# Optimization experiments

Hardware: AMD Instinct MI355X
Metric: run time of the kernel (lower is better)

## Reference

```python
import jax, jax.numpy as jnp
import numpy as np

TEMPERATURE = 0.07
EPS = 1e-8  # torch CosineSimilarity eps


def setup_inputs() -> dict:
    key = jax.random.key(0)
    k1, k2, k3 = jax.random.split(key, 3)
    N, D = 8192, 512
    features = jax.random.normal(k1, (N, D), dtype=jnp.float32)
    positive_mask = jax.random.randint(k2, (N, N), 0, 2, dtype=jnp.int32)
    negative_mask = jax.random.randint(k3, (N, N), 0, 2, dtype=jnp.int32)
    return {"features": features, "positive_mask": positive_mask, "negative_mask": negative_mask}


def reference(features, positive_mask, negative_mask):
    N = positive_mask.shape[0]
    self_contrast = 1.0 - jnp.eye(N, dtype=features.dtype)  # zero diagonal
    pos = positive_mask.astype(features.dtype) * self_contrast  # [N, N]
    neg = negative_mask.astype(features.dtype) * self_contrast  # [N, N]

    # cosine similarity via normalized matmul (same math as broadcasted CosineSimilarity)
    norm = jnp.maximum(jnp.linalg.norm(features, axis=1, keepdims=True), EPS)
    fn = features / norm  # [N, D]
    sim = jnp.matmul(fn, fn.T) / TEMPERATURE  # [N, N]

    logits_max = jax.lax.stop_gradient(jnp.max(sim, axis=1, keepdims=True))
    e = jnp.exp(sim - logits_max)  # [N, N]

    positives = e * pos
    log_neg_sum = jnp.log(jnp.sum(e * neg, axis=1, keepdims=True))  # [N, 1]
    log_prob = positives - log_neg_sum  # [N, N] (faithful to source: exp-masked, not log)

    cardinal = jnp.sum(pos, axis=1)
    cardinal = jnp.where(cardinal == 0, 1.0, cardinal)
    log_prob_sum = jnp.sum(log_prob * pos, axis=1)
    loss = -log_prob_sum / cardinal
    return jnp.mean(loss)
```

## Files before the change

kernel.cpp:

```cpp
#include <hip/hip_runtime.h>
#include <hip/hip_bf16.h>
#include <math.h>

#define NN 8192
#define DD 512
#define INV_T 14.285714285714286f

typedef __attribute__((ext_vector_type(8))) short s16x8;
typedef __attribute__((ext_vector_type(4))) float f32x4;
typedef __attribute__((ext_vector_type(4))) int   i32x4;

__device__ __forceinline__ unsigned short f32_to_bf16(float f) {
  unsigned int u = __float_as_uint(f);
  u += 0x7FFFu + ((u >> 16) & 1u);
  return (unsigned short)(u >> 16);
}

__device__ __forceinline__ void async16(const void* g, void* l) {
  __builtin_amdgcn_global_load_lds((__attribute__((address_space(1))) void*)(void*)g,
                                   (__attribute__((address_space(3))) void*)l,
                                   16, 0, 0);
}

__global__ __launch_bounds__(256) void normalize_kernel(const float* __restrict__ f,
                                                        unsigned short* __restrict__ fnb) {
  const int wave = threadIdx.x >> 6;
  const int lane = threadIdx.x & 63;
  const int row  = blockIdx.x * 4 + wave;
  const float* src = f + (size_t)row * DD + lane * 8;
  float4 v0 = *(const float4*)src;
  float4 v1 = *(const float4*)(src + 4);
  float ss = v0.x*v0.x + v0.y*v0.y + v0.z*v0.z + v0.w*v0.w
           + v1.x*v1.x + v1.y*v1.y + v1.z*v1.z + v1.w*v1.w;
  #pragma unroll
  for (int o = 32; o; o >>= 1) ss += __shfl_xor(ss, o);
  const float r = 1.0f / fmaxf(sqrtf(ss), 1e-8f);
  ushort4 a, b;
  a.x = f32_to_bf16(v0.x * r); a.y = f32_to_bf16(v0.y * r);
  a.z = f32_to_bf16(v0.z * r); a.w = f32_to_bf16(v0.w * r);
  b.x = f32_to_bf16(v1.x * r); b.y = f32_to_bf16(v1.y * r);
  b.z = f32_to_bf16(v1.z * r); b.w = f32_to_bf16(v1.w * r);
  unsigned short* dst = fnb + (size_t)row * DD + lane * 8;
  *(ushort4*)dst = a;
  *(ushort4*)(dst + 4) = b;
}

__global__ __launch_bounds__(256, 3) void fused_kernel(const unsigned short* __restrict__ fnb,
                                                       const int* __restrict__ posm,
                                                       const int* __restrict__ negm,
                                                       float* __restrict__ Spos,
                                                       float* __restrict__ Sneg,
                                                       float* __restrict__ Pcnt) {
  const int bid = blockIdx.x;
  int bi = (int)(64.5 - sqrt(64.5 * 64.5 - 2.0 * (double)bid));
  while (64 * bi - bi * (bi - 1) / 2 > bid) --bi;
  while (64 * (bi + 1) - (bi + 1) * bi / 2 <= bid) ++bi;
  const int bj = bi + (bid - (64 * bi - bi * (bi - 1) / 2));
  const int I = bi * 128;
  const int J = bj * 128;
  const bool offdiag = (bi != bj);

  const int tid  = threadIdx.x;
  const int wave = tid >> 6;
  const int lane = tid & 63;
  const int wm = wave >> 1;
  const int wn = wave & 1;
  const int q   = lane >> 4;
  const int c16 = lane & 15;

  __shared__ alignas(16) unsigned short lA[128 * 32];
  __shared__ alignas(16) unsigned short lB[128 * 32];
  __shared__ float sacc[2][128][3];
  for (int t = tid; t < 2 * 128 * 3; t += 256) ((float*)sacc)[t] = 0.f;

  f32x4 acc[4][4];
  const f32x4 z4 = {0.f, 0.f, 0.f, 0.f};
  #pragma unroll
  for (int mt = 0; mt < 4; ++mt)
    #pragma unroll
    for (int nt = 0; nt < 4; ++nt) acc[mt][nt] = z4;

  for (int kk = 0; kk < DD / 32; ++kk) {
    const int k0 = kk * 32;
    #pragma unroll
    for (int c = 0; c < 2; ++c) {
      const int fidx = tid + c * 256;
      const int L    = fidx >> 2;
      const int p    = fidx & 3;
      const int csrc = (p ^ ((L >> 1) & 3)) & 3;
      async16(fnb + (size_t)(I + L) * DD + k0 + csrc * 8, (char*)lA + fidx * 16);
      const int gB = 4 * (L & 31) + (L >> 5);
      async16(fnb + (size_t)(J + gB) * DD + k0 + csrc * 8, (char*)lB + fidx * 16);
    }
    __syncthreads();

    s16x8 aF[4], bF[4];
    #pragma unroll
    for (int t = 0; t < 4; ++t) {
      const int arow = wm * 64 + t * 16 + c16;
      const int apos = (q ^ ((arow >> 1) & 3)) & 3;
      aF[t] = *(const s16x8*)((const char*)lA + arow * 64 + apos * 16);
      const int Lb = (wn * 16 + c16) | (t << 5);
      const int bpos = (q ^ ((Lb >> 1) & 3)) & 3;
      bF[t] = *(const s16x8*)((const char*)lB + Lb * 64 + bpos * 16);
    }
    #pragma unroll
    for (int mt = 0; mt < 4; ++mt)
      #pragma unroll
      for (int nt = 0; nt < 4; ++nt)
        acc[mt][nt] = __builtin_amdgcn_mfma_f32_16x16x32_bf16(aF[mt], bF[nt], acc[mt][nt], 0, 0, 0);
    __syncthreads();
  }

  #pragma unroll
  for (int mt = 0; mt < 4; ++mt)
    #pragma unroll
    for (int nt = 0; nt < 4; ++nt)
      #pragma unroll
      for (int r = 0; r < 4; ++r)
        acc[mt][nt][r] = __expf(acc[mt][nt][r] * INV_T - INV_T);

  const bool hasdiag = (bi == bj) && (wm == wn);
  const int cb = wn * 64 + 4 * c16;

  #pragma unroll
  for (int mt = 0; mt < 4; ++mt) {
    const int rl = wm * 64 + mt * 16 + q * 4;
    i32x4 pv[4], nv[4];
    #pragma unroll
    for (int r = 0; r < 4; ++r) {
      const size_t off = (size_t)(I + rl + r) * NN + J + cb;
      pv[r] = __builtin_nontemporal_load((const i32x4*)(posm + off));
      nv[r] = __builtin_nontemporal_load((const i32x4*)(negm + off));
    }
    #pragma unroll
    for (int r = 0; r < 4; ++r) {
      float dsp = 0.f, dsn = 0.f, dpc = 0.f;
      #pragma unroll
      for (int nt = 0; nt < 4; ++nt) {
        float pf = (float)pv[r][nt];
        float nf = (float)nv[r][nt];
        if (hasdiag && (rl + r == cb + nt)) { pf = 0.f; nf = 0.f; }
        const float e = acc[mt][nt][r];
        dsp = fmaf(e, pf, dsp);
        dsn = fmaf(e, nf, dsn);
        dpc += pf;
      }
      #pragma unroll
      for (int o = 1; o <= 8; o <<= 1) {
        dsp += __shfl_xor(dsp, o);
        dsn += __shfl_xor(dsn, o);
        dpc += __shfl_xor(dpc, o);
      }
      if (c16 == 0) {
        atomicAdd(&sacc[0][rl + r][0], dsp);
        atomicAdd(&sacc[0][rl + r][1], dsn);
        atomicAdd(&sacc[0][rl + r][2], dpc);
      }
    }
  }

  if (offdiag) {
    #pragma unroll
    for (int nt = 0; nt < 4; ++nt) {
      const int trl = cb + nt;
      i32x4 pv[4], nv[4];
      #pragma unroll
      for (int mt = 0; mt < 4; ++mt) {
        const size_t off = (size_t)(J + trl) * NN + I + wm * 64 + mt * 16 + q * 4;
        pv[mt] = __builtin_nontemporal_load((const i32x4*)(posm + off));
        nv[mt] = __builtin_nontemporal_load((const i32x4*)(negm + off));
      }
      float ts = 0.f, tn = 0.f, tp = 0.f;
      #pragma unroll
      for (int mt = 0; mt < 4; ++mt) {
        #pragma unroll
        for (int r = 0; r < 4; ++r) {
          const float e = acc[mt][nt][r];
          ts = fmaf(e, (float)pv[mt][r], ts);
          tn = fmaf(e, (float)nv[mt][r], tn);
          tp += (float)pv[mt][r];
        }
      }
      ts += __shfl_xor(ts, 16); ts += __shfl_xor(ts, 32);
      tn += __shfl_xor(tn, 16); tn += __shfl_xor(tn, 32);
      tp += __shfl_xor(tp, 16); tp += __shfl_xor(tp, 32);
      if (q == 0) {
        atomicAdd(&sacc[1][trl][0], ts);
        atomicAdd(&sacc[1][trl][1], tn);
        atomicAdd(&sacc[1][trl][2], tp);
      }
    }
  }

  __syncthreads();

  const int r = tid & 127;
  if (tid < 128) {
    atomicAdd(&Spos[I + r], sacc[0][r][0]);
    atomicAdd(&Sneg[I + r], sacc[0][r][1]);
    atomicAdd(&Pcnt[I + r], sacc[0][r][2]);
  } else if (offdiag) {
    atomicAdd(&Spos[J + r], sacc[1][r][0]);
    atomicAdd(&Sneg[J + r], sacc[1][r][1]);
    atomicAdd(&Pcnt[J + r], sacc[1][r][2]);
  }
}

__global__ __launch_bounds__(256) void finalize_kernel(const float* __restrict__ Spos,
                                                       const float* __restrict__ Sneg,
                                                       const float* __restrict__ Pcnt,
                                                       float* __restrict__ out) {
  float local = 0.f;
  for (int i = threadIdx.x; i < NN; i += 256) {
    const float sp = Spos[i], sn = Sneg[i], pc = Pcnt[i];
    const float card = (pc == 0.f) ? 1.f : pc;
    local += (logf(sn) * pc - sp) / card;
  }
  #pragma unroll
  for (int o = 32; o; o >>= 1) local += __shfl_xor(local, o);
  __shared__ float red[4];
  if ((threadIdx.x & 63) == 0) red[threadIdx.x >> 6] = local;
  __syncthreads();
  if (threadIdx.x == 0)
    out[0] = (red[0] + red[1] + red[2] + red[3]) * (1.0f / (float)NN);
}

extern "C" void kernel_launch(void* const* d_in, const int* in_sizes, int n_in,
                              void* d_out, int out_size, void* d_ws, size_t ws_size,
                              hipStream_t stream) {
  const float* feat = (const float*)d_in[0];
  const int* posm   = (const int*)d_in[1];
  const int* negm   = (const int*)d_in[2];
  float* out = (float*)d_out;

  char* ws = (char*)d_ws;
  unsigned short* fnb = (unsigned short*)ws;
  float* Spos = (float*)(ws + (size_t)8 * 1024 * 1024);
  float* Sneg = Spos + NN;
  float* Pcnt = Sneg + NN;

  hipMemsetAsync(Spos, 0, 3 * NN * sizeof(float), stream);
  normalize_kernel<<<NN / 4, 256, 0, stream>>>(feat, fnb);
  fused_kernel<<<2080, 256, 0, stream>>>(fnb, posm, negm, Spos, Sneg, Pcnt);
  finalize_kernel<<<1, 256, 0, stream>>>(Spos, Sneg, Pcnt, out);
}
```

Before: 548.2 us.

## Raise occupancy by cutting register pressure, pipelining B fragments, folding memset

Launch bounds of the fused kernel go from 3 to 4 waves per SIMD. To fit, the B-fragment loads become a one-ahead software pipeline inside the MFMA loop, and the mask loads in both epilogues are split into two halves so fewer mask vectors are live at once. The separate memset is dropped, and the accumulator zeroing is folded into the normalize kernel. The workload is bound by mask bandwidth, so the extra occupancy may help hide latency, but the smaller load batches reduce memory-level parallelism per wave and may cause spills.

```diff
diff --git a/kernel.cpp b/kernel.cpp
--- a/kernel.cpp
+++ b/kernel.cpp
@@ -23,7 +23,10 @@
 }
 
 __global__ __launch_bounds__(256) void normalize_kernel(const float* __restrict__ f,
-                                                        unsigned short* __restrict__ fnb) {
+                                                        unsigned short* __restrict__ fnb,
+                                                        float* __restrict__ acc) {
+  if (blockIdx.x < 96) acc[blockIdx.x * 256 + threadIdx.x] = 0.f;
+
   const int wave = threadIdx.x >> 6;
   const int lane = threadIdx.x & 63;
   const int row  = blockIdx.x * 4 + wave;
@@ -45,7 +48,7 @@
   *(ushort4*)(dst + 4) = b;
 }
 
-__global__ __launch_bounds__(256, 3) void fused_kernel(const unsigned short* __restrict__ fnb,
+__global__ __launch_bounds__(256, 4) void fused_kernel(const unsigned short* __restrict__ fnb,
                                                        const int* __restrict__ posm,
                                                        const int* __restrict__ negm,
                                                        float* __restrict__ Spos,
@@ -94,21 +97,31 @@
     }
     __syncthreads();
 
-    s16x8 aF[4], bF[4];
+    s16x8 aF[4];
     #pragma unroll
     for (int t = 0; t < 4; ++t) {
       const int arow = wm * 64 + t * 16 + c16;
       const int apos = (q ^ ((arow >> 1) & 3)) & 3;
       aF[t] = *(const s16x8*)((const char*)lA + arow * 64 + apos * 16);
-      const int Lb = (wn * 16 + c16) | (t << 5);
+    }
+    s16x8 bcur, bnxt;
+    {
+      const int Lb = (wn * 16 + c16);
       const int bpos = (q ^ ((Lb >> 1) & 3)) & 3;
-      bF[t] = *(const s16x8*)((const char*)lB + Lb * 64 + bpos * 16);
-    }
-    #pragma unroll
-    for (int mt = 0; mt < 4; ++mt)
-      #pragma unroll
-      for (int nt = 0; nt < 4; ++nt)
-        acc[mt][nt] = __builtin_amdgcn_mfma_f32_16x16x32_bf16(aF[mt], bF[nt], acc[mt][nt], 0, 0, 0);
+      bcur = *(const s16x8*)((const char*)lB + Lb * 64 + bpos * 16);
+    }
+    #pragma unroll
+    for (int nt = 0; nt < 4; ++nt) {
+      if (nt < 3) {
+        const int Lb = (wn * 16 + c16) | ((nt + 1) << 5);
+        const int bpos = (q ^ ((Lb >> 1) & 3)) & 3;
+        bnxt = *(const s16x8*)((const char*)lB + Lb * 64 + bpos * 16);
+      }
+      #pragma unroll
+      for (int mt = 0; mt < 4; ++mt)
+        acc[mt][nt] = __builtin_amdgcn_mfma_f32_16x16x32_bf16(aF[mt], bcur, acc[mt][nt], 0, 0, 0);
+      bcur = bnxt;
+    }
     __syncthreads();
   }
 
@@ -126,36 +139,41 @@
   #pragma unroll
   for (int mt = 0; mt < 4; ++mt) {
     const int rl = wm * 64 + mt * 16 + q * 4;
-    i32x4 pv[4], nv[4];
-    #pragma unroll
-    for (int r = 0; r < 4; ++r) {
-      const size_t off = (size_t)(I + rl + r) * NN + J + cb;
-      pv[r] = __builtin_nontemporal_load((const i32x4*)(posm + off));
-      nv[r] = __builtin_nontemporal_load((const i32x4*)(negm + off));
-    }
-    #pragma unroll
-    for (int r = 0; r < 4; ++r) {
-      float dsp = 0.f, dsn = 0.f, dpc = 0.f;
-      #pragma unroll
-      for (int nt = 0; nt < 4; ++nt) {
-        float pf = (float)pv[r][nt];
-        float nf = (float)nv[r][nt];
-        if (hasdiag && (rl + r == cb + nt)) { pf = 0.f; nf = 0.f; }
-        const float e = acc[mt][nt][r];
-        dsp = fmaf(e, pf, dsp);
-        dsn = fmaf(e, nf, dsn);
-        dpc += pf;
-      }
-      #pragma unroll
-      for (int o = 1; o <= 8; o <<= 1) {
-        dsp += __shfl_xor(dsp, o);
-        dsn += __shfl_xor(dsn, o);
-        dpc += __shfl_xor(dpc, o);
-      }
-      if (c16 == 0) {
-        atomicAdd(&sacc[0][rl + r][0], dsp);
-        atomicAdd(&sacc[0][rl + r][1], dsn);
-        atomicAdd(&sacc[0][rl + r][2], dpc);
+    #pragma unroll
+    for (int h = 0; h < 2; ++h) {
+      i32x4 pv[2], nv[2];
+      #pragma unroll
+      for (int u = 0; u < 2; ++u) {
+        const int r = 2 * h + u;
+        const size_t off = (size_t)(I + rl + r) * NN + J + cb;
+        pv[u] = __builtin_nontemporal_load((const i32x4*)(posm + off));
+        nv[u] = __builtin_nontemporal_load((const i32x4*)(negm + off));
+      }
+      #pragma unroll
+      for (int u = 0; u < 2; ++u) {
+        const int r = 2 * h + u;
+        float dsp = 0.f, dsn = 0.f, dpc = 0.f;
+        #pragma unroll
+        for (int nt = 0; nt < 4; ++nt) {
+          float pf = (float)pv[u][nt];
+          float nf = (float)nv[u][nt];
+          if (hasdiag && (rl + r == cb + nt)) { pf = 0.f; nf = 0.f; }
+          const float e = acc[mt][nt][r];
+          dsp = fmaf(e, pf, dsp);
+          dsn = fmaf(e, nf, dsn);
+          dpc += pf;
+        }
+        #pragma unroll
+        for (int o = 1; o <= 8; o <<= 1) {
+          dsp += __shfl_xor(dsp, o);
+          dsn += __shfl_xor(dsn, o);
+          dpc += __shfl_xor(dpc, o);
+        }
+        if (c16 == 0) {
+          atomicAdd(&sacc[0][rl + r][0], dsp);
+          atomicAdd(&sacc[0][rl + r][1], dsn);
+          atomicAdd(&sacc[0][rl + r][2], dpc);
+        }
       }
     }
   }
@@ -164,22 +182,27 @@
     #pragma unroll
     for (int nt = 0; nt < 4; ++nt) {
       const int trl = cb + nt;
-      i32x4 pv[4], nv[4];
-      #pragma unroll
-      for (int mt = 0; mt < 4; ++mt) {
-        const size_t off = (size_t)(J + trl) * NN + I + wm * 64 + mt * 16 + q * 4;
-        pv[mt] = __builtin_nontemporal_load((const i32x4*)(posm + off));
-        nv[mt] = __builtin_nontemporal_load((const i32x4*)(negm + off));
-      }
       float ts = 0.f, tn = 0.f, tp = 0.f;
       #pragma unroll
-      for (int mt = 0; mt < 4; ++mt) {
-        #pragma unroll
-        for (int r = 0; r < 4; ++r) {
-          const float e = acc[mt][nt][r];
-          ts = fmaf(e, (float)pv[mt][r], ts);
-          tn = fmaf(e, (float)nv[mt][r], tn);
-          tp += (float)pv[mt][r];
+      for (int h = 0; h < 2; ++h) {
+        i32x4 pv[2], nv[2];
+        #pragma unroll
+        for (int u = 0; u < 2; ++u) {
+          const int mt = 2 * h + u;
+          const size_t off = (size_t)(J + trl) * NN + I + wm * 64 + mt * 16 + q * 4;
+          pv[u] = __builtin_nontemporal_load((const i32x4*)(posm + off));
+          nv[u] = __builtin_nontemporal_load((const i32x4*)(negm + off));
+        }
+        #pragma unroll
+        for (int u = 0; u < 2; ++u) {
+          const int mt = 2 * h + u;
+          #pragma unroll
+          for (int r = 0; r < 4; ++r) {
+            const float e = acc[mt][nt][r];
+            ts = fmaf(e, (float)pv[u][r], ts);
+            tn = fmaf(e, (float)nv[u][r], tn);
+            tp += (float)pv[u][r];
+          }
         }
       }
       ts += __shfl_xor(ts, 16); ts += __shfl_xor(ts, 32);
@@ -240,8 +263,7 @@
   float* Sneg = Spos + NN;
   float* Pcnt = Sneg + NN;
 
-  hipMemsetAsync(Spos, 0, 3 * NN * sizeof(float), stream);
-  normalize_kernel<<<NN / 4, 256, 0, stream>>>(feat, fnb);
+  normalize_kernel<<<NN / 4, 256, 0, stream>>>(feat, fnb, Spos);
   fused_kernel<<<2080, 256, 0, stream>>>(fnb, posm, negm, Spos, Sneg, Pcnt);
   finalize_kernel<<<1, 256, 0, stream>>>(Spos, Sneg, Pcnt, out);
 }
```

After: 584.4 us. +6.6%, slower.
